# Performance work log

Hardware: AMD Instinct MI355X
Metric: run time of the kernel (lower is better)

## Reference

```python
import jax, jax.numpy as jnp
import numpy as np

D_MODEL = 1024
D_INNER = 2048
N_EXPERTS = 8
TOP_K = 2
INIT_STD = 0.02


def setup_inputs() -> dict:
    key = jax.random.key(0)
    ks = jax.random.split(key, 6)
    B, S = 2, 2048
    x = jax.random.normal(ks[0], (B, S, D_MODEL), dtype=jnp.float32)
    router_w = jax.random.normal(ks[1], (N_EXPERTS, D_MODEL), dtype=jnp.float32) * (INIT_STD * 0.1)
    router_b = jnp.zeros((N_EXPERTS,), dtype=jnp.float32)
    gate_w = jax.random.normal(ks[2], (N_EXPERTS, D_MODEL, D_INNER), dtype=jnp.float32) * INIT_STD
    up_w = jax.random.normal(ks[3], (N_EXPERTS, D_MODEL, D_INNER), dtype=jnp.float32) * INIT_STD
    down_w = jax.random.normal(ks[4], (N_EXPERTS, D_INNER, D_MODEL), dtype=jnp.float32) * INIT_STD
    return {"x": x, "router_w": router_w, "router_b": router_b,
            "gate_w": gate_w, "up_w": up_w, "down_w": down_w}


def reference(x, router_w, router_b, gate_w, up_w, down_w):
    # Router: softmax over experts, top-k, renormalize top-k probs.
    logits = jnp.einsum('bsd,ed->bse', x, router_w) + router_b          # [B,S,E]
    probs = jax.nn.softmax(logits, axis=-1)
    top_p, top_i = jax.lax.top_k(probs, TOP_K)                           # [B,S,K]
    top_p = top_p / jnp.sum(top_p, axis=-1, keepdims=True)
    # Per-expert combine weight: c[b,s,e] = sum_k top_p[b,s,k] * [top_i[b,s,k]==e]
    onehot = jax.nn.one_hot(top_i, N_EXPERTS, dtype=x.dtype)             # [B,S,K,E]
    combine = jnp.einsum('bsk,bske->bse', top_p, onehot)                 # [B,S,E]
    # SwiGLU FFN for every expert (dense form of the masked dispatch),
    # zeroed/weighted by combine coefficients.
    g = jnp.einsum('bsd,edf->ebsf', x, gate_w)                           # [E,B,S,F]
    u = jnp.einsum('bsd,edf->ebsf', x, up_w)
    h = jax.nn.silu(g) * u
    y = jnp.einsum('ebsf,efd->ebsd', h, down_w)                          # [E,B,S,D]
    out = jnp.einsum('ebsd,bse->bsd', y, combine)
    return out
```

## Files before the change

kernel.cpp:

```cpp
#include <hip/hip_runtime.h>
#include <hip/hip_bf16.h>
#include <stdint.h>

#define D_MODEL 1024
#define D_INNER 2048
#define NEXP 8
#define TOPK 2
#define T256 40
#define T128 72

typedef float f32x4 __attribute__((ext_vector_type(4)));
typedef short bf16x8 __attribute__((ext_vector_type(8)));

#define MEMFENCE asm volatile("" ::: "memory")
#define SB __builtin_amdgcn_sched_barrier(0)
#define LGKM0 asm volatile("s_waitcnt lgkmcnt(0)" ::: "memory")
#define VM0 asm volatile("s_waitcnt vmcnt(0)" ::: "memory")
#define VM6 asm volatile("s_waitcnt vmcnt(6)" ::: "memory")
#define BAR __builtin_amdgcn_s_barrier()

#define Q8(I0, J0, AF, BF)                                                        \
  _Pragma("unroll") for (int i_ = 0; i_ < 2; i_++)                                \
    _Pragma("unroll") for (int j_ = 0; j_ < 2; j_++) {                            \
      acc[(I0) + i_][(J0) + j_] = __builtin_amdgcn_mfma_f32_16x16x32_bf16(        \
          AF[2 * i_], BF[2 * j_], acc[(I0) + i_][(J0) + j_], 0, 0, 0);            \
      acc[(I0) + i_][(J0) + j_] = __builtin_amdgcn_mfma_f32_16x16x32_bf16(        \
          AF[2 * i_ + 1], BF[2 * j_ + 1], acc[(I0) + i_][(J0) + j_], 0, 0, 0);    \
    }

__device__ __forceinline__ unsigned short f2b(float f) {
    union { float f; uint32_t u; } v; v.f = f;
    uint32_t u = v.u;
    return (unsigned short)((u + 0x7fffu + ((u >> 16) & 1u)) >> 16);
}

__device__ __forceinline__ void gl_lds16(const void* g, void* l) {
    __builtin_amdgcn_global_load_lds((const __attribute__((address_space(1))) void*)g,
                                     (__attribute__((address_space(3))) void*)l, 16, 0, 0);
}

__global__ __launch_bounds__(256) void tcast3_kernel(
    const float* __restrict__ gw, const float* __restrict__ uw, const float* __restrict__ dw,
    unsigned short* __restrict__ gT, unsigned short* __restrict__ uT, unsigned short* __restrict__ dT)
{
    __shared__ unsigned short S[64][68];
    int which = blockIdx.z >> 3;
    int e = blockIdx.z & 7;
    const float* in; unsigned short* out; int K, N;
    if (which == 0)      { in = gw; out = gT; K = D_MODEL; N = D_INNER; }
    else if (which == 1) { in = uw; out = uT; K = D_MODEL; N = D_INNER; }
    else                 { in = dw; out = dT; K = D_INNER; N = D_MODEL; }
    int n0 = blockIdx.x * 64, k0 = blockIdx.y * 64;
    if (n0 >= N || k0 >= K) return;
    const float* ib = in + (size_t)e * K * N;
    unsigned short* ob = out + (size_t)e * N * K;
    int tid = threadIdx.x;
    int kk = tid >> 4, nn4 = (tid & 15) * 4;
#pragma unroll
    for (int j = 0; j < 4; j++) {
        int k = kk + 16 * j;
        float4 v = *(const float4*)&ib[(size_t)(k0 + k) * N + n0 + nn4];
        ushort4 s; s.x = f2b(v.x); s.y = f2b(v.y); s.z = f2b(v.z); s.w = f2b(v.w);
        *(ushort4*)&S[k][nn4] = s;
    }
    __syncthreads();
    int nn = tid >> 4, kk4 = (tid & 15) * 4;
#pragma unroll
    for (int j = 0; j < 4; j++) {
        int n = nn + 16 * j;
        ushort4 s;
        s.x = S[kk4 + 0][n]; s.y = S[kk4 + 1][n];
        s.z = S[kk4 + 2][n]; s.w = S[kk4 + 3][n];
        *(ushort4*)&ob[(size_t)(n0 + n) * K + k0 + kk4] = s;
    }
}

__global__ __launch_bounds__(64) void router_kernel(
    const float* __restrict__ x, const float* __restrict__ rw,
    const float* __restrict__ rb, unsigned short* __restrict__ xb,
    int* __restrict__ top_i, float* __restrict__ top_w, int T)
{
    int t = blockIdx.x;
    if (t >= T) return;
    int l = threadIdx.x;
    float xv[16];
#pragma unroll
    for (int i = 0; i < 16; i++) xv[i] = x[(size_t)t * D_MODEL + l + 64 * i];
#pragma unroll
    for (int i = 0; i < 16; i++) xb[(size_t)t * D_MODEL + l + 64 * i] = f2b(xv[i]);
    float logit[NEXP];
#pragma unroll
    for (int e = 0; e < NEXP; e++) {
        float acc = 0.f;
#pragma unroll
        for (int i = 0; i < 16; i++) acc += xv[i] * rw[e * D_MODEL + l + 64 * i];
#pragma unroll
        for (int s = 32; s > 0; s >>= 1) acc += __shfl_xor(acc, s, 64);
        logit[e] = acc + rb[e];
    }
    if (l == 0) {
        int i0 = 0; float m0 = logit[0];
#pragma unroll
        for (int e = 1; e < NEXP; e++) if (logit[e] > m0) { m0 = logit[e]; i0 = e; }
        int i1 = -1; float m1 = -3.0e38f;
#pragma unroll
        for (int e = 0; e < NEXP; e++) {
            if (e == i0) continue;
            if (logit[e] > m1) { m1 = logit[e]; i1 = e; }
        }
        float w0 = 1.f / (1.f + expf(m1 - m0));
        top_i[t * 2 + 0] = i0; top_i[t * 2 + 1] = i1;
        top_w[t * 2 + 0] = w0; top_w[t * 2 + 1] = 1.f - w0;
    }
}

__global__ __launch_bounds__(256) void bucket_kernel(
    const int* __restrict__ top_i, const float* __restrict__ top_w,
    int* __restrict__ meta, int* __restrict__ tok_of_slot,
    float* __restrict__ w_of_slot, int T)
{
    __shared__ int cnt[256][NEXP];
    __shared__ int pre[256][NEXP];
    __shared__ int tot[NEXP];
    __shared__ int off[NEXP + 1];
    int tid = threadIdx.x;
    int per = (T + 255) / 256;
    int t0 = tid * per;
    for (int e = 0; e < NEXP; e++) cnt[tid][e] = 0;
    for (int t = t0; t < t0 + per && t < T; t++)
        for (int k = 0; k < TOPK; k++) cnt[tid][top_i[t * 2 + k]]++;
    __syncthreads();
    if (tid < NEXP) {
        int run = 0;
        for (int i = 0; i < 256; i++) { pre[i][tid] = run; run += cnt[i][tid]; }
        tot[tid] = run;
    }
    __syncthreads();
    if (tid == 0) {
        off[0] = 0;
        for (int e = 0; e < NEXP; e++) off[e + 1] = off[e] + tot[e];
        for (int e = 0; e <= NEXP; e++) meta[e] = off[e];
        int nt = 0;
        for (int e = 0; e < NEXP; e++)
            for (int r = off[e]; r < off[e + 1]; r += 256)
                meta[16 + nt++] = (e << 16) | r;
        meta[11] = nt;
        for (; nt < T256; nt++) meta[16 + nt] = -1;
        nt = 0;
        for (int e = 0; e < NEXP; e++)
            for (int r = off[e]; r < off[e + 1]; r += 128)
                meta[64 + nt++] = (e << 16) | r;
        meta[12] = nt;
        for (; nt < T128; nt++) meta[64 + nt] = -1;
    }
    __syncthreads();
    int lc[NEXP];
#pragma unroll
    for (int e = 0; e < NEXP; e++) lc[e] = 0;
    for (int t = t0; t < t0 + per && t < T; t++) {
        for (int k = 0; k < TOPK; k++) {
            int e = top_i[t * 2 + k];
            int slot = off[e] + pre[tid][e] + lc[e]++;
            tok_of_slot[slot] = t;
            w_of_slot[slot] = top_w[t * 2 + k];
        }
    }
}

__global__ __launch_bounds__(512, 2) void moe_gate_up(
    const unsigned short* __restrict__ xb, const unsigned short* __restrict__ wgT,
    const unsigned short* __restrict__ wuT, const int* __restrict__ meta,
    const int* __restrict__ tok_of_slot, unsigned short* __restrict__ H)
{
    extern __shared__ __align__(16) unsigned short lds[];

    int lin = blockIdx.x;
    int strip = (lin & 7) * 4 + ((lin >> 3) & 3);
    int tix = lin >> 5;
    int packed = meta[16 + tix];
    if (packed < 0) return;
    int e = packed >> 16, row0 = packed & 0xffff;
    int Mloc = min(256, meta[e + 1] - row0);
    int f0 = strip * 64;

    int tid = threadIdx.x, wv = tid >> 6, lane = tid & 63;
    int lrow = lane & 15, kgrp = lane >> 4, sw = lrow & 7;
    int mh = wv >> 1, sel = wv & 1;
    int co0 = 8 * (kgrp ^ sw);
    int co1 = 8 * ((4 + kgrp) ^ sw);

    int srow = tid >> 3, schk = tid & 7;
    const unsigned short* sA[4];
#pragma unroll
    for (int j = 0; j < 4; j++) {
        int r = j * 64 + srow;
        int slot = row0 + ((r < Mloc) ? r : 0);
        sA[j] = xb + (size_t)tok_of_slot[slot] * D_MODEL + 8 * (schk ^ (r & 7));
    }
    const unsigned short *sG, *sU;
    {
        size_t wb = (size_t)e * D_MODEL * D_INNER + (size_t)(f0 + srow) * D_MODEL + 8 * (schk ^ (srow & 7));
        sG = wgT + wb; sU = wuT + wb;
    }
    int dst = tid * 8;

    int aoff[4], boff[4];
#pragma unroll
    for (int i = 0; i < 4; i++) aoff[i] = (mh * 64 + i * 16 + lrow) * 64;
    int bb = 16384 + sel * 4096;
#pragma unroll
    for (int i = 0; i < 4; i++) boff[i] = bb + (i * 16 + lrow) * 64;

    f32x4 acc[4][4];
#pragma unroll
    for (int i = 0; i < 4; i++)
#pragma unroll
        for (int j = 0; j < 4; j++) acc[i][j] = (f32x4){0.f, 0.f, 0.f, 0.f};

    auto stageA01 = [&](int u) {
        int kk = u * 64; unsigned short* b = lds + (u % 3) * 24576;
        gl_lds16(sA[0] + kk, b + dst);
        gl_lds16(sA[1] + kk, b + 4096 + dst);
    };
    auto stageA23 = [&](int u) {
        int kk = u * 64; unsigned short* b = lds + (u % 3) * 24576;
        gl_lds16(sA[2] + kk, b + 8192 + dst);
        gl_lds16(sA[3] + kk, b + 12288 + dst);
    };
    auto stageGU = [&](int u) {
        int kk = u * 64; unsigned short* b = lds + (u % 3) * 24576;
        gl_lds16(sG + kk, b + 16384 + dst);
        gl_lds16(sU + kk, b + 20480 + dst);
    };

    bf16x8 A0[4], A1[4], B0[4], B1[4];

    const int NT = D_MODEL / 64;
    stageA01(0); stageA23(0); stageGU(0);
    stageA01(1); stageA23(1); stageGU(1);
    MEMFENCE; VM6; BAR; MEMFENCE;

    for (int t = 0; t < NT; ++t) {
        const unsigned short* b = lds + (t % 3) * 24576;
        bool pf = (t + 2) < NT;
        A0[0] = *(const bf16x8*)(b + aoff[0] + co0);
        A0[1] = *(const bf16x8*)(b + aoff[0] + co1);
        A0[2] = *(const bf16x8*)(b + aoff[1] + co0);
        A0[3] = *(const bf16x8*)(b + aoff[1] + co1);
        B0[0] = *(const bf16x8*)(b + boff[0] + co0);
        B0[1] = *(const bf16x8*)(b + boff[0] + co1);
        B0[2] = *(const bf16x8*)(b + boff[1] + co0);
        B0[3] = *(const bf16x8*)(b + boff[1] + co1);
        if (pf) stageA01(t + 2);
        SB; BAR; LGKM0; SB;
        __builtin_amdgcn_s_setprio(1); Q8(0, 0, A0, B0); __builtin_amdgcn_s_setprio(0);
        SB; BAR;
        B1[0] = *(const bf16x8*)(b + boff[2] + co0);
        B1[1] = *(const bf16x8*)(b + boff[2] + co1);
        B1[2] = *(const bf16x8*)(b + boff[3] + co0);
        B1[3] = *(const bf16x8*)(b + boff[3] + co1);
        if (pf) stageA23(t + 2);
        SB; BAR; LGKM0; SB;
        __builtin_amdgcn_s_setprio(1); Q8(0, 2, A0, B1); __builtin_amdgcn_s_setprio(0);
        SB; BAR;
        A1[0] = *(const bf16x8*)(b + aoff[2] + co0);
        A1[1] = *(const bf16x8*)(b + aoff[2] + co1);
        A1[2] = *(const bf16x8*)(b + aoff[3] + co0);
        A1[3] = *(const bf16x8*)(b + aoff[3] + co1);
        if (pf) stageGU(t + 2);
        SB; BAR; LGKM0; SB;
        __builtin_amdgcn_s_setprio(1); Q8(2, 0, A1, B0); __builtin_amdgcn_s_setprio(0);
        SB; BAR;
        __builtin_amdgcn_s_setprio(1); Q8(2, 2, A1, B1); __builtin_amdgcn_s_setprio(0);
        SB;
        if (pf) { VM6; } else { VM0; }
        BAR; MEMFENCE;
    }

    __syncthreads();
    float* ex = (float*)lds;
    if (sel == 1) {
        float* d = ex + mh * 4160;
#pragma unroll
        for (int i = 0; i < 4; i++)
#pragma unroll
            for (int j = 0; j < 4; j++)
#pragma unroll
                for (int r = 0; r < 4; r++)
                    d[(i * 16 + kgrp * 4 + r) * 65 + j * 16 + lrow] = acc[i][j][r];
    }
    __syncthreads();
    if (sel == 0) {
        const float* s = ex + mh * 4160;
#pragma unroll
        for (int i = 0; i < 4; i++)
#pragma unroll
            for (int j = 0; j < 4; j++)
#pragma unroll
                for (int r = 0; r < 4; r++) {
                    int row = i * 16 + kgrp * 4 + r;
                    int m = mh * 64 + row;
                    if (m < Mloc) {
                        float g = acc[i][j][r];
                        float u = s[row * 65 + j * 16 + lrow];
                        float h = g / (1.f + __expf(-g)) * u;
                        H[(size_t)(row0 + m) * D_INNER + f0 + j * 16 + lrow] = f2b(h);
                    }
                }
    }
}

__global__ __launch_bounds__(512, 2) void moe_down(
    const unsigned short* __restrict__ H, const unsigned short* __restrict__ wdT,
    const int* __restrict__ meta, const int* __restrict__ tok_of_slot,
    const float* __restrict__ w_of_slot, float* __restrict__ out, int S2)
{
    extern __shared__ __align__(16) unsigned short lds[];
    __shared__ int toks[128];
    __shared__ float wts[128];

    int lin = blockIdx.x;
    int dstrip = lin & 3;
    int kq = (lin >> 2) & 1;
    int tix = lin >> 3;
    int packed = meta[64 + tix];
    if (packed < 0) return;
    int e = packed >> 16, row0 = packed & 0xffff;
    int Mloc = min(128, meta[e + 1] - row0);
    int d0 = dstrip * 256;
    int kb = kq * 1024;

    int tid = threadIdx.x, wv = tid >> 6, lane = tid & 63;
    int lrow = lane & 15, kgrp = lane >> 4, sw = lrow & 7;
    int mh = wv >> 2, nh = wv & 3;
    int co0 = 8 * (kgrp ^ sw);
    int co1 = 8 * ((4 + kgrp) ^ sw);

    if (tid < 128) {
        bool v = tid < Mloc;
        toks[tid] = v ? tok_of_slot[row0 + tid] : 0;
        wts[tid] = v ? w_of_slot[row0 + tid] : 0.f;
    }

    int srow = tid >> 3, schk = tid & 7;
    const unsigned short* sA[2];
#pragma unroll
    for (int j = 0; j < 2; j++) {
        int r = j * 64 + srow;
        int slot = min(row0 + r, S2 - 1);
        sA[j] = H + (size_t)slot * D_INNER + kb + 8 * (schk ^ (r & 7));
    }
    const unsigned short* sB[4];
#pragma unroll
    for (int j = 0; j < 4; j++) {
        int r = j * 64 + srow;
        sB[j] = wdT + (size_t)e * D_INNER * D_MODEL + (size_t)(d0 + r) * D_INNER + kb + 8 * (schk ^ (r & 7));
    }
    int dst = tid * 8;

    int aoff[4], boff[4];
#pragma unroll
    for (int i = 0; i < 4; i++) aoff[i] = (mh * 64 + i * 16 + lrow) * 64;
#pragma unroll
    for (int i = 0; i < 4; i++) boff[i] = 8192 + (nh * 64 + i * 16 + lrow) * 64;

    f32x4 acc[4][4];
#pragma unroll
    for (int i = 0; i < 4; i++)
#pragma unroll
        for (int j = 0; j < 4; j++) acc[i][j] = (f32x4){0.f, 0.f, 0.f, 0.f};

    auto stageA = [&](int u) {
        int kk = u * 64; unsigned short* b = lds + (u % 3) * 24576;
        gl_lds16(sA[0] + kk, b + dst);
        gl_lds16(sA[1] + kk, b + 4096 + dst);
    };
    auto stageB01 = [&](int u) {
        int kk = u * 64; unsigned short* b = lds + (u % 3) * 24576;
        gl_lds16(sB[0] + kk, b + 8192 + dst);
        gl_lds16(sB[1] + kk, b + 12288 + dst);
    };
    auto stageB23 = [&](int u) {
        int kk = u * 64; unsigned short* b = lds + (u % 3) * 24576;
        gl_lds16(sB[2] + kk, b + 16384 + dst);
        gl_lds16(sB[3] + kk, b + 20480 + dst);
    };

    bf16x8 A0[4], A1[4], B0[4], B1[4];

    const int NT = 1024 / 64;
    stageA(0); stageB01(0); stageB23(0);
    stageA(1); stageB01(1); stageB23(1);
    MEMFENCE; VM6; BAR; MEMFENCE;

    for (int t = 0; t < NT; ++t) {
        const unsigned short* b = lds + (t % 3) * 24576;
        bool pf = (t + 2) < NT;
        A0[0] = *(const bf16x8*)(b + aoff[0] + co0);
        A0[1] = *(const bf16x8*)(b + aoff[0] + co1);
        A0[2] = *(const bf16x8*)(b + aoff[1] + co0);
        A0[3] = *(const bf16x8*)(b + aoff[1] + co1);
        B0[0] = *(const bf16x8*)(b + boff[0] + co0);
        B0[1] = *(const bf16x8*)(b + boff[0] + co1);
        B0[2] = *(const bf16x8*)(b + boff[1] + co0);
        B0[3] = *(const bf16x8*)(b + boff[1] + co1);
        if (pf) stageA(t + 2);
        SB; BAR; LGKM0; SB;
        __builtin_amdgcn_s_setprio(1); Q8(0, 0, A0, B0); __builtin_amdgcn_s_setprio(0);
        SB; BAR;
        B1[0] = *(const bf16x8*)(b + boff[2] + co0);
        B1[1] = *(const bf16x8*)(b + boff[2] + co1);
        B1[2] = *(const bf16x8*)(b + boff[3] + co0);
        B1[3] = *(const bf16x8*)(b + boff[3] + co1);
        if (pf) stageB01(t + 2);
        SB; BAR; LGKM0; SB;
        __builtin_amdgcn_s_setprio(1); Q8(0, 2, A0, B1); __builtin_amdgcn_s_setprio(0);
        SB; BAR;
        A1[0] = *(const bf16x8*)(b + aoff[2] + co0);
        A1[1] = *(const bf16x8*)(b + aoff[2] + co1);
        A1[2] = *(const bf16x8*)(b + aoff[3] + co0);
        A1[3] = *(const bf16x8*)(b + aoff[3] + co1);
        if (pf) stageB23(t + 2);
        SB; BAR; LGKM0; SB;
        __builtin_amdgcn_s_setprio(1); Q8(2, 0, A1, B0); __builtin_amdgcn_s_setprio(0);
        SB; BAR;
        __builtin_amdgcn_s_setprio(1); Q8(2, 2, A1, B1); __builtin_amdgcn_s_setprio(0);
        SB;
        if (pf) { VM6; } else { VM0; }
        BAR; MEMFENCE;
    }

#pragma unroll
    for (int i = 0; i < 4; i++)
#pragma unroll
        for (int j = 0; j < 4; j++)
#pragma unroll
            for (int r = 0; r < 4; r++) {
                int m = mh * 64 + i * 16 + kgrp * 4 + r;
                if (m < Mloc) {
                    int n = d0 + nh * 64 + j * 16 + lrow;
                    atomicAdd(&out[(size_t)toks[m] * D_MODEL + n], wts[m] * acc[i][j][r]);
                }
            }
}

extern "C" void kernel_launch(void* const* d_in, const int* in_sizes, int n_in,
                              void* d_out, int out_size, void* d_ws, size_t ws_size,
                              hipStream_t stream) {
    const float* x  = (const float*)d_in[0];
    const float* rw = (const float*)d_in[1];
    const float* rb = (const float*)d_in[2];
    const float* gw = (const float*)d_in[3];
    const float* uw = (const float*)d_in[4];
    const float* dw = (const float*)d_in[5];
    float* out = (float*)d_out;

    int T = in_sizes[0] / D_MODEL;
    int S2 = 2 * T;

    char* ws = (char*)d_ws;
    size_t cur = 0;
    auto take = [&](size_t bytes) { char* p = ws + cur; cur = (cur + bytes + 255) & ~(size_t)255; return p; };
    int*   top_i = (int*)take((size_t)S2 * 4);
    float* top_w = (float*)take((size_t)S2 * 4);
    int*   meta  = (int*)take(1024);
    int*   tos   = (int*)take((size_t)S2 * 4);
    float* wos   = (float*)take((size_t)S2 * 4);
    unsigned short* xb  = (unsigned short*)take((size_t)T * D_MODEL * 2);
    unsigned short* wgT = (unsigned short*)take((size_t)NEXP * D_MODEL * D_INNER * 2);
    unsigned short* wuT = (unsigned short*)take((size_t)NEXP * D_MODEL * D_INNER * 2);
    unsigned short* wdT = (unsigned short*)take((size_t)NEXP * D_MODEL * D_INNER * 2);
    unsigned short* H   = (unsigned short*)take((size_t)S2 * D_INNER * 2);

    static const int RING_LDS = 3 * 24576 * 2;
    hipFuncSetAttribute((const void*)moe_gate_up,
                        hipFuncAttributeMaxDynamicSharedMemorySize, RING_LDS);
    hipFuncSetAttribute((const void*)moe_down,
                        hipFuncAttributeMaxDynamicSharedMemorySize, RING_LDS);

    hipMemsetAsync(d_out, 0, (size_t)out_size * sizeof(float), stream);

    tcast3_kernel<<<dim3(32, 32, 24), 256, 0, stream>>>(gw, uw, dw, wgT, wuT, wdT);
    router_kernel<<<T, 64, 0, stream>>>(x, rw, rb, xb, top_i, top_w, T);
    bucket_kernel<<<1, 256, 0, stream>>>(top_i, top_w, meta, tos, wos, T);

    moe_gate_up<<<T256 * 32, 512, RING_LDS, stream>>>(xb, wgT, wuT, meta, tos, H);
    moe_down<<<T128 * 8, 512, RING_LDS, stream>>>(H, wdT, meta, tos, wos, out, S2);
}
```

Measured before the change: 315.4 us.

## Retile down projection to 256x128 full-K tiles and simplify MFMA pipelines

The down kernel moves from 128-row tiles with a split-K of two (1024 each) to 256-row by 128-column tiles covering the full 2048 K. This halves the atomic accumulations into the output and reuses the gate-up tile metadata. Both GEMM kernels replace the hand-interleaved four-phase LDS-read/MFMA schedule with two simpler phases, drop the sched_barrier and lgkmcnt waits, and change launch bounds from 2 to 1 waves per SIMD. The exchange-buffer stride changes from 65 to 66. Risks are fewer blocks in the down kernel, lower occupancy hints, and weaker latency hiding without the explicit scheduling barriers.

```diff
diff --git a/kernel.cpp b/kernel.cpp
--- a/kernel.cpp
+++ b/kernel.cpp
@@ -12,21 +12,9 @@
 typedef float f32x4 __attribute__((ext_vector_type(4)));
 typedef short bf16x8 __attribute__((ext_vector_type(8)));
 
-#define MEMFENCE asm volatile("" ::: "memory")
-#define SB __builtin_amdgcn_sched_barrier(0)
-#define LGKM0 asm volatile("s_waitcnt lgkmcnt(0)" ::: "memory")
 #define VM0 asm volatile("s_waitcnt vmcnt(0)" ::: "memory")
 #define VM6 asm volatile("s_waitcnt vmcnt(6)" ::: "memory")
 #define BAR __builtin_amdgcn_s_barrier()
-
-#define Q8(I0, J0, AF, BF)                                                        \
-  _Pragma("unroll") for (int i_ = 0; i_ < 2; i_++)                                \
-    _Pragma("unroll") for (int j_ = 0; j_ < 2; j_++) {                            \
-      acc[(I0) + i_][(J0) + j_] = __builtin_amdgcn_mfma_f32_16x16x32_bf16(        \
-          AF[2 * i_], BF[2 * j_], acc[(I0) + i_][(J0) + j_], 0, 0, 0);            \
-      acc[(I0) + i_][(J0) + j_] = __builtin_amdgcn_mfma_f32_16x16x32_bf16(        \
-          AF[2 * i_ + 1], BF[2 * j_ + 1], acc[(I0) + i_][(J0) + j_], 0, 0, 0);    \
-    }
 
 __device__ __forceinline__ unsigned short f2b(float f) {
     union { float f; uint32_t u; } v; v.f = f;
@@ -146,12 +134,6 @@
                 meta[16 + nt++] = (e << 16) | r;
         meta[11] = nt;
         for (; nt < T256; nt++) meta[16 + nt] = -1;
-        nt = 0;
-        for (int e = 0; e < NEXP; e++)
-            for (int r = off[e]; r < off[e + 1]; r += 128)
-                meta[64 + nt++] = (e << 16) | r;
-        meta[12] = nt;
-        for (; nt < T128; nt++) meta[64 + nt] = -1;
     }
     __syncthreads();
     int lc[NEXP];
@@ -167,7 +149,7 @@
     }
 }
 
-__global__ __launch_bounds__(512, 2) void moe_gate_up(
+__global__ __launch_bounds__(512, 1) void moe_gate_up(
     const unsigned short* __restrict__ xb, const unsigned short* __restrict__ wgT,
     const unsigned short* __restrict__ wuT, const int* __restrict__ meta,
     const int* __restrict__ tok_of_slot, unsigned short* __restrict__ H)
@@ -185,7 +167,7 @@
 
     int tid = threadIdx.x, wv = tid >> 6, lane = tid & 63;
     int lrow = lane & 15, kgrp = lane >> 4, sw = lrow & 7;
-    int mh = wv >> 1, sel = wv & 1;
+    int wm = wv >> 1, sel = wv & 1;
     int co0 = 8 * (kgrp ^ sw);
     int co1 = 8 * ((4 + kgrp) ^ sw);
 
@@ -206,10 +188,9 @@
 
     int aoff[4], boff[4];
 #pragma unroll
-    for (int i = 0; i < 4; i++) aoff[i] = (mh * 64 + i * 16 + lrow) * 64;
-    int bb = 16384 + sel * 4096;
-#pragma unroll
-    for (int i = 0; i < 4; i++) boff[i] = bb + (i * 16 + lrow) * 64;
+    for (int i = 0; i < 4; i++) aoff[i] = (wm * 64 + i * 16 + lrow) * 64;
+#pragma unroll
+    for (int i = 0; i < 4; i++) boff[i] = 16384 + (sel * 64 + i * 16 + lrow) * 64;
 
     f32x4 acc[4][4];
 #pragma unroll
@@ -217,81 +198,84 @@
 #pragma unroll
         for (int j = 0; j < 4; j++) acc[i][j] = (f32x4){0.f, 0.f, 0.f, 0.f};
 
-    auto stageA01 = [&](int u) {
+    auto stageA = [&](int u) {
         int kk = u * 64; unsigned short* b = lds + (u % 3) * 24576;
         gl_lds16(sA[0] + kk, b + dst);
         gl_lds16(sA[1] + kk, b + 4096 + dst);
-    };
-    auto stageA23 = [&](int u) {
-        int kk = u * 64; unsigned short* b = lds + (u % 3) * 24576;
         gl_lds16(sA[2] + kk, b + 8192 + dst);
         gl_lds16(sA[3] + kk, b + 12288 + dst);
     };
-    auto stageGU = [&](int u) {
+    auto stageB = [&](int u) {
         int kk = u * 64; unsigned short* b = lds + (u % 3) * 24576;
         gl_lds16(sG + kk, b + 16384 + dst);
         gl_lds16(sU + kk, b + 20480 + dst);
     };
 
-    bf16x8 A0[4], A1[4], B0[4], B1[4];
-
     const int NT = D_MODEL / 64;
-    stageA01(0); stageA23(0); stageGU(0);
-    stageA01(1); stageA23(1); stageGU(1);
-    MEMFENCE; VM6; BAR; MEMFENCE;
+    stageA(0); stageB(0); stageA(1); stageB(1);
+    VM6; BAR;
 
     for (int t = 0; t < NT; ++t) {
         const unsigned short* b = lds + (t % 3) * 24576;
         bool pf = (t + 2) < NT;
-        A0[0] = *(const bf16x8*)(b + aoff[0] + co0);
-        A0[1] = *(const bf16x8*)(b + aoff[0] + co1);
-        A0[2] = *(const bf16x8*)(b + aoff[1] + co0);
-        A0[3] = *(const bf16x8*)(b + aoff[1] + co1);
-        B0[0] = *(const bf16x8*)(b + boff[0] + co0);
-        B0[1] = *(const bf16x8*)(b + boff[0] + co1);
-        B0[2] = *(const bf16x8*)(b + boff[1] + co0);
-        B0[3] = *(const bf16x8*)(b + boff[1] + co1);
-        if (pf) stageA01(t + 2);
-        SB; BAR; LGKM0; SB;
-        __builtin_amdgcn_s_setprio(1); Q8(0, 0, A0, B0); __builtin_amdgcn_s_setprio(0);
-        SB; BAR;
-        B1[0] = *(const bf16x8*)(b + boff[2] + co0);
-        B1[1] = *(const bf16x8*)(b + boff[2] + co1);
-        B1[2] = *(const bf16x8*)(b + boff[3] + co0);
-        B1[3] = *(const bf16x8*)(b + boff[3] + co1);
-        if (pf) stageA23(t + 2);
-        SB; BAR; LGKM0; SB;
-        __builtin_amdgcn_s_setprio(1); Q8(0, 2, A0, B1); __builtin_amdgcn_s_setprio(0);
-        SB; BAR;
-        A1[0] = *(const bf16x8*)(b + aoff[2] + co0);
-        A1[1] = *(const bf16x8*)(b + aoff[2] + co1);
-        A1[2] = *(const bf16x8*)(b + aoff[3] + co0);
-        A1[3] = *(const bf16x8*)(b + aoff[3] + co1);
-        if (pf) stageGU(t + 2);
-        SB; BAR; LGKM0; SB;
-        __builtin_amdgcn_s_setprio(1); Q8(2, 0, A1, B0); __builtin_amdgcn_s_setprio(0);
-        SB; BAR;
-        __builtin_amdgcn_s_setprio(1); Q8(2, 2, A1, B1); __builtin_amdgcn_s_setprio(0);
-        SB;
+        bf16x8 A[4][2], B[2][2];
+#pragma unroll
+        for (int i = 0; i < 4; i++) {
+            A[i][0] = *(const bf16x8*)(b + aoff[i] + co0);
+            A[i][1] = *(const bf16x8*)(b + aoff[i] + co1);
+        }
+#pragma unroll
+        for (int j = 0; j < 2; j++) {
+            B[j][0] = *(const bf16x8*)(b + boff[j] + co0);
+            B[j][1] = *(const bf16x8*)(b + boff[j] + co1);
+        }
+        if (pf) stageA(t + 2);
+        BAR;
+        __builtin_amdgcn_s_setprio(1);
+#pragma unroll
+        for (int i = 0; i < 4; i++)
+#pragma unroll
+            for (int j = 0; j < 2; j++) {
+                acc[i][j] = __builtin_amdgcn_mfma_f32_16x16x32_bf16(A[i][0], B[j][0], acc[i][j], 0, 0, 0);
+                acc[i][j] = __builtin_amdgcn_mfma_f32_16x16x32_bf16(A[i][1], B[j][1], acc[i][j], 0, 0, 0);
+            }
+        __builtin_amdgcn_s_setprio(0);
+        BAR;
+#pragma unroll
+        for (int j = 0; j < 2; j++) {
+            B[j][0] = *(const bf16x8*)(b + boff[2 + j] + co0);
+            B[j][1] = *(const bf16x8*)(b + boff[2 + j] + co1);
+        }
+        if (pf) stageB(t + 2);
+        BAR;
+        __builtin_amdgcn_s_setprio(1);
+#pragma unroll
+        for (int i = 0; i < 4; i++)
+#pragma unroll
+            for (int j = 0; j < 2; j++) {
+                acc[i][2 + j] = __builtin_amdgcn_mfma_f32_16x16x32_bf16(A[i][0], B[j][0], acc[i][2 + j], 0, 0, 0);
+                acc[i][2 + j] = __builtin_amdgcn_mfma_f32_16x16x32_bf16(A[i][1], B[j][1], acc[i][2 + j], 0, 0, 0);
+            }
+        __builtin_amdgcn_s_setprio(0);
         if (pf) { VM6; } else { VM0; }
-        BAR; MEMFENCE;
+        BAR;
     }
 
     __syncthreads();
     float* ex = (float*)lds;
     if (sel == 1) {
-        float* d = ex + mh * 4160;
+        float* d = ex + wm * 4224;
 #pragma unroll
         for (int i = 0; i < 4; i++)
 #pragma unroll
             for (int j = 0; j < 4; j++)
 #pragma unroll
                 for (int r = 0; r < 4; r++)
-                    d[(i * 16 + kgrp * 4 + r) * 65 + j * 16 + lrow] = acc[i][j][r];
+                    d[(i * 16 + kgrp * 4 + r) * 66 + j * 16 + lrow] = acc[i][j][r];
     }
     __syncthreads();
     if (sel == 0) {
-        const float* s = ex + mh * 4160;
+        const float* s = ex + wm * 4224;
 #pragma unroll
         for (int i = 0; i < 4; i++)
 #pragma unroll
@@ -299,10 +283,10 @@
 #pragma unroll
                 for (int r = 0; r < 4; r++) {
                     int row = i * 16 + kgrp * 4 + r;
-                    int m = mh * 64 + row;
+                    int m = wm * 64 + row;
                     if (m < Mloc) {
                         float g = acc[i][j][r];
-                        float u = s[row * 65 + j * 16 + lrow];
+                        float u = s[row * 66 + j * 16 + lrow];
                         float h = g / (1.f + __expf(-g)) * u;
                         H[(size_t)(row0 + m) * D_INNER + f0 + j * 16 + lrow] = f2b(h);
                     }
@@ -310,59 +294,56 @@
     }
 }
 
-__global__ __launch_bounds__(512, 2) void moe_down(
+__global__ __launch_bounds__(512, 1) void moe_down(
     const unsigned short* __restrict__ H, const unsigned short* __restrict__ wdT,
     const int* __restrict__ meta, const int* __restrict__ tok_of_slot,
-    const float* __restrict__ w_of_slot, float* __restrict__ out, int S2)
+    const float* __restrict__ w_of_slot, float* __restrict__ out)
 {
     extern __shared__ __align__(16) unsigned short lds[];
-    __shared__ int toks[128];
-    __shared__ float wts[128];
+    __shared__ int toks[256];
+    __shared__ float wts[256];
 
     int lin = blockIdx.x;
-    int dstrip = lin & 3;
-    int kq = (lin >> 2) & 1;
+    int d0 = (lin & 7) * 128;
     int tix = lin >> 3;
-    int packed = meta[64 + tix];
+    int packed = meta[16 + tix];
     if (packed < 0) return;
     int e = packed >> 16, row0 = packed & 0xffff;
-    int Mloc = min(128, meta[e + 1] - row0);
-    int d0 = dstrip * 256;
-    int kb = kq * 1024;
+    int Mloc = min(256, meta[e + 1] - row0);
 
     int tid = threadIdx.x, wv = tid >> 6, lane = tid & 63;
     int lrow = lane & 15, kgrp = lane >> 4, sw = lrow & 7;
-    int mh = wv >> 2, nh = wv & 3;
+    int wm = wv >> 1, wn = wv & 1;
     int co0 = 8 * (kgrp ^ sw);
     int co1 = 8 * ((4 + kgrp) ^ sw);
 
-    if (tid < 128) {
+    if (tid < 256) {
         bool v = tid < Mloc;
         toks[tid] = v ? tok_of_slot[row0 + tid] : 0;
         wts[tid] = v ? w_of_slot[row0 + tid] : 0.f;
     }
 
     int srow = tid >> 3, schk = tid & 7;
-    const unsigned short* sA[2];
+    const unsigned short* sA[4];
+#pragma unroll
+    for (int j = 0; j < 4; j++) {
+        int r = j * 64 + srow;
+        int slot = row0 + ((r < Mloc) ? r : 0);
+        sA[j] = H + (size_t)slot * D_INNER + 8 * (schk ^ (r & 7));
+    }
+    const unsigned short* sB[2];
 #pragma unroll
     for (int j = 0; j < 2; j++) {
         int r = j * 64 + srow;
-        int slot = min(row0 + r, S2 - 1);
-        sA[j] = H + (size_t)slot * D_INNER + kb + 8 * (schk ^ (r & 7));
-    }
-    const unsigned short* sB[4];
-#pragma unroll
-    for (int j = 0; j < 4; j++) {
-        int r = j * 64 + srow;
-        sB[j] = wdT + (size_t)e * D_INNER * D_MODEL + (size_t)(d0 + r) * D_INNER + kb + 8 * (schk ^ (r & 7));
+        sB[j] = wdT + (size_t)e * D_INNER * D_MODEL + (size_t)(d0 + r) * D_INNER + 8 * (schk ^ (r & 7));
     }
     int dst = tid * 8;
 
     int aoff[4], boff[4];
 #pragma unroll
-    for (int i = 0; i < 4; i++) aoff[i] = (mh * 64 + i * 16 + lrow) * 64;
-#pragma unroll
-    for (int i = 0; i < 4; i++) boff[i] = 8192 + (nh * 64 + i * 16 + lrow) * 64;
+    for (int i = 0; i < 4; i++) aoff[i] = (wm * 64 + i * 16 + lrow) * 64;
+#pragma unroll
+    for (int i = 0; i < 4; i++) boff[i] = 16384 + (wn * 64 + i * 16 + lrow) * 64;
 
     f32x4 acc[4][4];
 #pragma unroll
@@ -374,60 +355,63 @@
         int kk = u * 64; unsigned short* b = lds + (u % 3) * 24576;
         gl_lds16(sA[0] + kk, b + dst);
         gl_lds16(sA[1] + kk, b + 4096 + dst);
+        gl_lds16(sA[2] + kk, b + 8192 + dst);
+        gl_lds16(sA[3] + kk, b + 12288 + dst);
     };
-    auto stageB01 = [&](int u) {
+    auto stageB = [&](int u) {
         int kk = u * 64; unsigned short* b = lds + (u % 3) * 24576;
-        gl_lds16(sB[0] + kk, b + 8192 + dst);
-        gl_lds16(sB[1] + kk, b + 12288 + dst);
+        gl_lds16(sB[0] + kk, b + 16384 + dst);
+        gl_lds16(sB[1] + kk, b + 20480 + dst);
     };
-    auto stageB23 = [&](int u) {
-        int kk = u * 64; unsigned short* b = lds + (u % 3) * 24576;
-        gl_lds16(sB[2] + kk, b + 16384 + dst);
-        gl_lds16(sB[3] + kk, b + 20480 + dst);
-    };
-
-    bf16x8 A0[4], A1[4], B0[4], B1[4];
-
-    const int NT = 1024 / 64;
-    stageA(0); stageB01(0); stageB23(0);
-    stageA(1); stageB01(1); stageB23(1);
-    MEMFENCE; VM6; BAR; MEMFENCE;
+
+    const int NT = D_INNER / 64;
+    stageA(0); stageB(0); stageA(1); stageB(1);
+    VM6; BAR;
 
     for (int t = 0; t < NT; ++t) {
         const unsigned short* b = lds + (t % 3) * 24576;
         bool pf = (t + 2) < NT;
-        A0[0] = *(const bf16x8*)(b + aoff[0] + co0);
-        A0[1] = *(const bf16x8*)(b + aoff[0] + co1);
-        A0[2] = *(const bf16x8*)(b + aoff[1] + co0);
-        A0[3] = *(const bf16x8*)(b + aoff[1] + co1);
-        B0[0] = *(const bf16x8*)(b + boff[0] + co0);
-        B0[1] = *(const bf16x8*)(b + boff[0] + co1);
-        B0[2] = *(const bf16x8*)(b + boff[1] + co0);
-        B0[3] = *(const bf16x8*)(b + boff[1] + co1);
+        bf16x8 A[4][2], B[2][2];
+#pragma unroll
+        for (int i = 0; i < 4; i++) {
+            A[i][0] = *(const bf16x8*)(b + aoff[i] + co0);
+            A[i][1] = *(const bf16x8*)(b + aoff[i] + co1);
+        }
+#pragma unroll
+        for (int j = 0; j < 2; j++) {
+            B[j][0] = *(const bf16x8*)(b + boff[j] + co0);
+            B[j][1] = *(const bf16x8*)(b + boff[j] + co1);
+        }
         if (pf) stageA(t + 2);
-        SB; BAR; LGKM0; SB;
-        __builtin_amdgcn_s_setprio(1); Q8(0, 0, A0, B0); __builtin_amdgcn_s_setprio(0);
-        SB; BAR;
-        B1[0] = *(const bf16x8*)(b + boff[2] + co0);
-        B1[1] = *(const bf16x8*)(b + boff[2] + co1);
-        B1[2] = *(const bf16x8*)(b + boff[3] + co0);
-        B1[3] = *(const bf16x8*)(b + boff[3] + co1);
-        if (pf) stageB01(t + 2);
-        SB; BAR; LGKM0; SB;
-        __builtin_amdgcn_s_setprio(1); Q8(0, 2, A0, B1); __builtin_amdgcn_s_setprio(0);
-        SB; BAR;
-        A1[0] = *(const bf16x8*)(b + aoff[2] + co0);
-        A1[1] = *(const bf16x8*)(b + aoff[2] + co1);
-        A1[2] = *(const bf16x8*)(b + aoff[3] + co0);
-        A1[3] = *(const bf16x8*)(b + aoff[3] + co1);
-        if (pf) stageB23(t + 2);
-        SB; BAR; LGKM0; SB;
-        __builtin_amdgcn_s_setprio(1); Q8(2, 0, A1, B0); __builtin_amdgcn_s_setprio(0);
-        SB; BAR;
-        __builtin_amdgcn_s_setprio(1); Q8(2, 2, A1, B1); __builtin_amdgcn_s_setprio(0);
-        SB;
+        BAR;
+        __builtin_amdgcn_s_setprio(1);
+#pragma unroll
+        for (int i = 0; i < 4; i++)
+#pragma unroll
+            for (int j = 0; j < 2; j++) {
+                acc[i][j] = __builtin_amdgcn_mfma_f32_16x16x32_bf16(A[i][0], B[j][0], acc[i][j], 0, 0, 0);
+                acc[i][j] = __builtin_amdgcn_mfma_f32_16x16x32_bf16(A[i][1], B[j][1], acc[i][j], 0, 0, 0);
+            }
+        __builtin_amdgcn_s_setprio(0);
+        BAR;
+#pragma unroll
+        for (int j = 0; j < 2; j++) {
+            B[j][0] = *(const bf16x8*)(b + boff[2 + j] + co0);
+            B[j][1] = *(const bf16x8*)(b + boff[2 + j] + co1);
+        }
+        if (pf) stageB(t + 2);
+        BAR;
+        __builtin_amdgcn_s_setprio(1);
+#pragma unroll
+        for (int i = 0; i < 4; i++)
+#pragma unroll
+            for (int j = 0; j < 2; j++) {
+                acc[i][2 + j] = __builtin_amdgcn_mfma_f32_16x16x32_bf16(A[i][0], B[j][0], acc[i][2 + j], 0, 0, 0);
+                acc[i][2 + j] = __builtin_amdgcn_mfma_f32_16x16x32_bf16(A[i][1], B[j][1], acc[i][2 + j], 0, 0, 0);
+            }
+        __builtin_amdgcn_s_setprio(0);
         if (pf) { VM6; } else { VM0; }
-        BAR; MEMFENCE;
+        BAR;
     }
 
 #pragma unroll
@@ -436,9 +420,9 @@
         for (int j = 0; j < 4; j++)
 #pragma unroll
             for (int r = 0; r < 4; r++) {
-                int m = mh * 64 + i * 16 + kgrp * 4 + r;
+                int m = wm * 64 + i * 16 + kgrp * 4 + r;
                 if (m < Mloc) {
-                    int n = d0 + nh * 64 + j * 16 + lrow;
+                    int n = d0 + wn * 64 + j * 16 + lrow;
                     atomicAdd(&out[(size_t)toks[m] * D_MODEL + n], wts[m] * acc[i][j][r]);
                 }
             }
@@ -485,5 +469,5 @@
     bucket_kernel<<<1, 256, 0, stream>>>(top_i, top_w, meta, tos, wos, T);
 
     moe_gate_up<<<T256 * 32, 512, RING_LDS, stream>>>(xb, wgT, wuT, meta, tos, H);
-    moe_down<<<T128 * 8, 512, RING_LDS, stream>>>(H, wdT, meta, tos, wos, out, S2);
-}
+    moe_down<<<T256 * 8, 512, RING_LDS, stream>>>(H, wdT, meta, tos, wos, out);
+}
```

Result: faster. 300.2 us (-4.8%).
